# Performance work log

Measured on AMD Instinct MI355X. Metric: run time of the kernel, lower is better.

## Reference

```python
import jax, jax.numpy as jnp
import numpy as np

N, E = 50000, 800000
IN, HID, OUT, H = 128, 16, 16, 4


def setup_inputs() -> dict:
    key = jax.random.key(0)
    ks = jax.random.split(key, 11)
    sc = 0.1
    return {
        "features": jax.random.normal(ks[0], (N, IN), jnp.float32),
        "src": jax.random.randint(ks[1], (E,), 0, N, dtype=jnp.int64) if jax.config.jax_enable_x64 else jax.random.randint(ks[1], (E,), 0, N).astype(jnp.int32),
        "dst": jax.random.randint(ks[2], (E,), 0, N).astype(jnp.int32),
        "W1": jax.random.normal(ks[3], (H * HID, IN), jnp.float32) * sc,
        "al1": jax.random.normal(ks[4], (H, HID), jnp.float32) * sc,
        "ar1": jax.random.normal(ks[5], (H, HID), jnp.float32) * sc,
        "b1": jax.random.normal(ks[6], (H * HID,), jnp.float32) * sc,
        "W2": jax.random.normal(ks[7], (H * OUT, H * HID), jnp.float32) * sc,
        "al2": jax.random.normal(ks[8], (H, OUT), jnp.float32) * sc,
        "ar2": jax.random.normal(ks[9], (H, OUT), jnp.float32) * sc,
        "b2": jax.random.normal(ks[10], (H * OUT,), jnp.float32) * sc,
    }


def gat_conv(src, dst, feat, W, al, ar, b, heads, dout):
    """DGL-style GATConv: fc -> edge attention -> dst-softmax -> scatter-sum."""
    n = feat.shape[0]
    h = (feat @ W.T).reshape(n, heads, dout)            # [N,H,D]
    el = jnp.einsum("nhd,hd->nh", h, al)                # [N,H]
    er = jnp.einsum("nhd,hd->nh", h, ar)                # [N,H]
    e = jax.nn.leaky_relu(el[src] + er[dst], 0.2)       # [E,H]
    m = jax.ops.segment_max(e, dst, num_segments=n)     # per-dst max, [N,H]
    a = jnp.exp(e - m[dst])                             # [E,H]
    s = jax.ops.segment_sum(a, dst, num_segments=n)     # [N,H]
    alpha = a / s[dst]                                  # edge softmax, [E,H]
    out = jax.ops.segment_sum(alpha[:, :, None] * h[src], dst, num_segments=n)
    return out + b.reshape(1, heads, dout)              # [N,H,D]


def reference(features, src, dst, W1, al1, ar1, b1, W2, al2, ar2, b2):
    h = gat_conv(src, dst, features, W1, al1, ar1, b1, H, HID).reshape(N, H * HID)
    h = jax.nn.relu(h)
    h = gat_conv(src, dst, h, W2, al2, ar2, b2, H, OUT).mean(axis=1)  # mean over heads
    return jax.nn.log_softmax(h, axis=1)
```

## Files before the change

kernel.cpp:

```cpp
#include <hip/hip_runtime.h>
#include <math.h>

#define N_NODES 50000
#define N_EDGES 800000
#define NPART 8
#define PART_SZ ((N_NODES + NPART - 1) / NPART)
#define CAP 64
#define SCAT_BLOCKS 4096

typedef __attribute__((ext_vector_type(8))) short short8;
typedef __attribute__((ext_vector_type(8))) unsigned short ushort8;
typedef __attribute__((ext_vector_type(4))) float v4f;
typedef __attribute__((ext_vector_type(2))) float v2f;
typedef __attribute__((ext_vector_type(4))) int int4v;

__device__ __forceinline__ float bf2f(unsigned short h) {
    return __uint_as_float(((unsigned int)h) << 16);
}
__device__ __forceinline__ unsigned short f2bf(float f) {
    unsigned int u = __float_as_uint(f);
    u += 0x7fff + ((u >> 16) & 1);
    return (unsigned short)(u >> 16);
}

__device__ __forceinline__ short8 load_afrag(const float* X, size_t row, int K,
                                             int kc, int quad) {
    const float* p = X + row * K + kc * 32 + quad * 8;
    const float4 t0 = *(const float4*)p;
    const float4 t1 = *(const float4*)(p + 4);
    short8 a;
    a[0] = (short)f2bf(t0.x); a[1] = (short)f2bf(t0.y);
    a[2] = (short)f2bf(t0.z); a[3] = (short)f2bf(t0.w);
    a[4] = (short)f2bf(t1.x); a[5] = (short)f2bf(t1.y);
    a[6] = (short)f2bf(t1.z); a[7] = (short)f2bf(t1.w);
    return a;
}
__device__ __forceinline__ short8 load_afrag(const unsigned short* X, size_t row,
                                             int K, int kc, int quad) {
    return *(const short8*)(X + row * K + kc * 32 + quad * 8);
}

template <int K, typename XT>
__global__ __launch_bounds__(256) void fc_att_mfma(
    const XT* __restrict__ X, const float* __restrict__ W,
    const float* __restrict__ al, const float* __restrict__ ar,
    unsigned short* __restrict__ Hout, float* __restrict__ el,
    float* __restrict__ er, int nTiles)
{
    constexpr int KP = K + 4;
    constexpr int NKC = K / 32;
    __shared__ float Wlds[64 * KP];
    const int tid = threadIdx.x;
    for (int i = tid; i < 64 * K; i += 256) {
        int r = i / K, c = i - r * K;
        Wlds[r * KP + c] = W[i];
    }
    __syncthreads();

    const int lane = tid & 63;
    const int wave = tid >> 6;
    const int d = lane & 15;
    const int quad = lane >> 4;

    short8 wf[4][NKC];
#pragma unroll
    for (int ng = 0; ng < 4; ++ng) {
#pragma unroll
        for (int kc = 0; kc < NKC; ++kc) {
            const float* wp = &Wlds[(ng * 16 + d) * KP + kc * 32 + quad * 8];
            const v4f w0 = *(const v4f*)wp;
            const v4f w1 = *(const v4f*)(wp + 4);
            short8 f;
            f[0] = (short)f2bf(w0[0]); f[1] = (short)f2bf(w0[1]);
            f[2] = (short)f2bf(w0[2]); f[3] = (short)f2bf(w0[3]);
            f[4] = (short)f2bf(w1[0]); f[5] = (short)f2bf(w1[1]);
            f[6] = (short)f2bf(w1[2]); f[7] = (short)f2bf(w1[3]);
            wf[ng][kc] = f;
        }
    }

    const int tile = blockIdx.x * 4 + wave;
    if (tile >= nTiles) return;
    const int node0 = tile * 16;

    v4f cc[4] = {{0.f,0.f,0.f,0.f},{0.f,0.f,0.f,0.f},{0.f,0.f,0.f,0.f},{0.f,0.f,0.f,0.f}};
#pragma unroll
    for (int kc = 0; kc < NKC; ++kc) {
        const short8 a = load_afrag(X, (size_t)(node0 + d), K, kc, quad);
        cc[0] = __builtin_amdgcn_mfma_f32_16x16x32_bf16(a, wf[0][kc], cc[0], 0, 0, 0);
        cc[1] = __builtin_amdgcn_mfma_f32_16x16x32_bf16(a, wf[1][kc], cc[1], 0, 0, 0);
        cc[2] = __builtin_amdgcn_mfma_f32_16x16x32_bf16(a, wf[2][kc], cc[2], 0, 0, 0);
        cc[3] = __builtin_amdgcn_mfma_f32_16x16x32_bf16(a, wf[3][kc], cc[3], 0, 0, 0);
    }

#pragma unroll
    for (int ng = 0; ng < 4; ++ng) {
        const float alv = al[ng * 16 + d];
        const float arv = ar[ng * 16 + d];
        const v4f c = cc[ng];
#pragma unroll
        for (int r = 0; r < 4; ++r) {
            const int node = node0 + quad * 4 + r;
            Hout[(size_t)node * 64 + ng * 16 + d] = f2bf(c[r]);
            float vel = c[r] * alv;
            float ver = c[r] * arv;
#pragma unroll
            for (int off = 1; off < 16; off <<= 1) {
                vel += __shfl_xor(vel, off);
                ver += __shfl_xor(ver, off);
            }
            if (d == 0) {
                el[node * 4 + ng] = vel;
                er[node * 4 + ng] = ver;
            }
        }
    }
}

__device__ __forceinline__ void scat1(int d, int s, int lo, int hi,
                                      int* __restrict__ cnt16,
                                      unsigned short* __restrict__ col)
{
    if (d >= lo && d < hi) {
        const int pos = atomicAdd(&cnt16[(unsigned)d * 16], 1);
        if (pos < CAP) col[(unsigned)d * CAP + pos] = (unsigned short)s;
    }
}

__global__ __launch_bounds__(256) void scatter_bucket_kernel(
    const int* __restrict__ src, const int* __restrict__ dst,
    int* __restrict__ cnt16, unsigned short* __restrict__ col)
{
    const int part = blockIdx.x & (NPART - 1);
    const int lo = part * PART_SZ;
    const int hi = lo + PART_SZ;
    const int tid_p = ((int)blockIdx.x >> 3) * 256 + threadIdx.x;
    const int stride = (SCAT_BLOCKS / NPART) * 256;
    const int4v* dst4 = (const int4v*)dst;
    const int4v* src4 = (const int4v*)src;
    const int NQ = N_EDGES / 4;
    for (int q = tid_p; q < NQ; q += 2 * stride) {
        const int q2 = q + stride;
        const bool ok2 = q2 < NQ;
        const int4v dA = __builtin_nontemporal_load(dst4 + q);
        const int4v sA = __builtin_nontemporal_load(src4 + q);
        const int4v dB = ok2 ? __builtin_nontemporal_load(dst4 + q2) : (int4v){-1,-1,-1,-1};
        const int4v sB = ok2 ? __builtin_nontemporal_load(src4 + q2) : (int4v){0,0,0,0};
        scat1(dA[0], sA[0], lo, hi, cnt16, col);
        scat1(dA[1], sA[1], lo, hi, cnt16, col);
        scat1(dA[2], sA[2], lo, hi, cnt16, col);
        scat1(dA[3], sA[3], lo, hi, cnt16, col);
        scat1(dB[0], sB[0], lo, hi, cnt16, col);
        scat1(dB[1], sB[1], lo, hi, cnt16, col);
        scat1(dB[2], sB[2], lo, hi, cnt16, col);
        scat1(dB[3], sB[3], lo, hi, cnt16, col);
    }
}

__device__ __forceinline__ void agg_walk_pair(
    const unsigned short* __restrict__ colrow, int len, int len_max,
    const float* __restrict__ el, const unsigned int* __restrict__ Hf32,
    int hb, int hl, float erv_a,
    float& accL_out, float& accH_out, float& sacc_a_out)
{
    const int j_a = hl >> 2;
    const unsigned h_a = (unsigned)(hl & 3);
    const int hd = hl >> 3;
    float accL0 = 0.f, accL1 = 0.f, accH0 = 0.f, accH1 = 0.f;
    float sacc_a = 0.f;
    for (int i = 0; i < len_max; i += 16) {
        const ushort8 sv0 = __builtin_nontemporal_load((const ushort8*)(colrow + i));
        const ushort8 sv1 = __builtin_nontemporal_load((const ushort8*)(colrow + i + 8));
        const int rm = len - i;
        const unsigned sa0 = (unsigned)colrow[i + j_a];
        const unsigned sa1 = (unsigned)colrow[i + 8 + j_a];
        float x0 = el[sa0 * 4u + h_a] + erv_a;
        float x1 = el[sa1 * 4u + h_a] + erv_a;
        x0 = fmaxf(x0, 0.2f * x0);
        x1 = fmaxf(x1, 0.2f * x1);
        float a0 = __expf(x0);
        float a1 = __expf(x1);
        a0 = (j_a < rm) ? a0 : 0.f;
        a1 = (j_a + 8 < rm) ? a1 : 0.f;
        sacc_a += a0 + a1;
        unsigned uu[16];
#pragma unroll
        for (int j = 0; j < 8; ++j)
            uu[j] = Hf32[(unsigned)sv0[j] * 32u + (unsigned)hl];
#pragma unroll
        for (int j = 0; j < 8; ++j)
            uu[8 + j] = Hf32[(unsigned)sv1[j] * 32u + (unsigned)hl];
#pragma unroll
        for (int j = 0; j < 8; ++j) {
            const float aj = __shfl(a0, hb + j * 4 + hd);
            const float lo = __uint_as_float(uu[j] << 16);
            const float hi = __uint_as_float(uu[j] & 0xffff0000u);
            if (j & 1) { accL1 = fmaf(aj, lo, accL1); accH1 = fmaf(aj, hi, accH1); }
            else       { accL0 = fmaf(aj, lo, accL0); accH0 = fmaf(aj, hi, accH0); }
        }
#pragma unroll
        for (int j = 0; j < 8; ++j) {
            const float aj = __shfl(a1, hb + j * 4 + hd);
            const float lo = __uint_as_float(uu[8 + j] << 16);
            const float hi = __uint_as_float(uu[8 + j] & 0xffff0000u);
            if (j & 1) { accL1 = fmaf(aj, lo, accL1); accH1 = fmaf(aj, hi, accH1); }
            else       { accL0 = fmaf(aj, lo, accL0); accH0 = fmaf(aj, hi, accH0); }
        }
    }
    sacc_a += __shfl_xor(sacc_a, 4);
    sacc_a += __shfl_xor(sacc_a, 8);
    sacc_a += __shfl_xor(sacc_a, 16);
    sacc_a_out = sacc_a;
    accL_out = accL0 + accL1;
    accH_out = accH0 + accH1;
}

__global__ __launch_bounds__(256) void agg_relu_kernel(
    const int* __restrict__ cnt16, const unsigned short* __restrict__ col,
    const float* __restrict__ el, const float* __restrict__ er,
    const unsigned int* __restrict__ Hf32, const float* __restrict__ b,
    unsigned int* __restrict__ out32, int n)
{
    const int lane = threadIdx.x & 63;
    const int wave = threadIdx.x >> 6;
    const int hl = lane & 31;
    const int hb = lane & 32;
    const int node = blockIdx.x * 8 + wave * 2 + (lane >> 5);
    if (node >= n) return;
    const int hd = hl >> 3;
    const int cg = hd * 16 + (hl & 7) * 2;
    const float erv_a = er[node * 4 + (hl & 3)];
    const int len = min(cnt16[(unsigned)node * 16], CAP);
    const int len_max = max(len, __shfl_xor(len, 32));
    float accL, accH, sacc_a;
    agg_walk_pair(col + (unsigned)node * CAP, len, len_max, el, Hf32,
                  hb, hl, erv_a, accL, accH, sacc_a);
    const float sc = __shfl(sacc_a, hb + hd);
    float vL = sc > 0.f ? accL / sc : 0.f;
    float vH = sc > 0.f ? accH / sc : 0.f;
    vL += b[cg];   vH += b[cg + 1];
    vL = vL > 0.f ? vL : 0.f;
    vH = vH > 0.f ? vH : 0.f;
    const unsigned u = (unsigned)f2bf(vL) | ((unsigned)f2bf(vH) << 16);
    __builtin_nontemporal_store(u, out32 + (size_t)node * 32 + hl);
}

__global__ __launch_bounds__(256) void agg_final_kernel(
    const int* __restrict__ cnt16, const unsigned short* __restrict__ col,
    const float* __restrict__ el, const float* __restrict__ er,
    const unsigned int* __restrict__ Hf32, const float* __restrict__ b,
    float* __restrict__ out, int n)
{
    const int lane = threadIdx.x & 63;
    const int wave = threadIdx.x >> 6;
    const int hl = lane & 31;
    const int hb = lane & 32;
    const int node = blockIdx.x * 8 + wave * 2 + (lane >> 5);
    if (node >= n) return;
    const int hd = hl >> 3;
    const int cg = hd * 16 + (hl & 7) * 2;
    const float erv_a = er[node * 4 + (hl & 3)];
    const int len = min(cnt16[(unsigned)node * 16], CAP);
    const int len_max = max(len, __shfl_xor(len, 32));
    float accL, accH, sacc_a;
    agg_walk_pair(col + (unsigned)node * CAP, len, len_max, el, Hf32,
                  hb, hl, erv_a, accL, accH, sacc_a);
    const float sc = __shfl(sacc_a, hb + hd);
    float zL = sc > 0.f ? accL / sc : 0.f;
    float zH = sc > 0.f ? accH / sc : 0.f;
    zL += b[cg];   zH += b[cg + 1];
    zL += __shfl_xor(zL, 8);  zL += __shfl_xor(zL, 16);  zL *= 0.25f;
    zH += __shfl_xor(zH, 8);  zH += __shfl_xor(zH, 16);  zH *= 0.25f;
    float m = fmaxf(zL, zH);
    m = fmaxf(m, __shfl_xor(m, 1));
    m = fmaxf(m, __shfl_xor(m, 2));
    m = fmaxf(m, __shfl_xor(m, 4));
    float se = __expf(zL - m) + __expf(zH - m);
    se += __shfl_xor(se, 1);
    se += __shfl_xor(se, 2);
    se += __shfl_xor(se, 4);
    const float lse = __logf(se);
    if (hl < 8) {
        v2f r;
        r[0] = zL - m - lse;
        r[1] = zH - m - lse;
        __builtin_nontemporal_store(r, (v2f*)(out + (size_t)node * 16 + hl * 2));
    }
}

extern "C" void kernel_launch(void* const* d_in, const int* in_sizes, int n_in,
                              void* d_out, int out_size, void* d_ws, size_t ws_size,
                              hipStream_t stream)
{
    const float* feat = (const float*)d_in[0];
    const int*   src  = (const int*)d_in[1];
    const int*   dst  = (const int*)d_in[2];
    const float* W1   = (const float*)d_in[3];
    const float* al1  = (const float*)d_in[4];
    const float* ar1  = (const float*)d_in[5];
    const float* b1   = (const float*)d_in[6];
    const float* W2   = (const float*)d_in[7];
    const float* al2  = (const float*)d_in[8];
    const float* ar2  = (const float*)d_in[9];
    const float* b2   = (const float*)d_in[10];
    float* out = (float*)d_out;

    float* el  = (float*)d_ws;
    float* er  = el + N_NODES * 4;
    int*   cnt16 = (int*)(er + N_NODES * 4);
    uintptr_t p = ((uintptr_t)(cnt16 + N_NODES * 16) + 15) & ~(uintptr_t)15;
    unsigned short* col = (unsigned short*)p;
    unsigned short* A   = col + (size_t)N_NODES * CAP + 64;
    unsigned short* B   = A + (size_t)N_NODES * 64;

    const int NT = N_NODES / 16;
    const int FB = (NT + 3) / 4;
    const int AB2 = (N_NODES + 7) / 8;

    (void)hipMemsetAsync(cnt16, 0, (size_t)((char*)A - (char*)cnt16), stream);
    scatter_bucket_kernel<<<SCAT_BLOCKS, 256, 0, stream>>>(src, dst, cnt16, col);

    fc_att_mfma<128, float><<<FB, 256, 0, stream>>>(feat, W1, al1, ar1, A, el, er, NT);
    agg_relu_kernel<<<AB2, 256, 0, stream>>>(cnt16, col, el, er,
                                             (const unsigned int*)A, b1,
                                             (unsigned int*)B, N_NODES);

    fc_att_mfma<64, unsigned short><<<FB, 256, 0, stream>>>(B, W2, al2, ar2, A, el, er, NT);
    agg_final_kernel<<<AB2, 256, 0, stream>>>(cnt16, col, el, er,
                                              (const unsigned int*)A, b2, out, N_NODES);
}
```

Baseline: 197.8 us.

## Fuse layer-1 FC matmul and edge bucketing into one heterogeneous launch

Merges the edge scatter/bucketing kernel and the first FC+attention MFMA kernel into a single launch, where the first 784 blocks do the matmul and the rest do scatter. The two are independent, so this lets the compute-bound FC overlap with the atomic-heavy scatter and removes one launch gap. The weight tile is also stored in shared memory as bf16 instead of fp32 and is read straight into fragments, with no per-wave conversion. The trade-off is that the scatter blocks now reserve the FC shared-memory allocation, which may lower their occupancy.

```diff
diff --git a/kernel.cpp b/kernel.cpp
--- a/kernel.cpp
+++ b/kernel.cpp
@@ -7,6 +7,7 @@
 #define PART_SZ ((N_NODES + NPART - 1) / NPART)
 #define CAP 64
 #define SCAT_BLOCKS 4096
+#define FC_BLOCKS 784
 
 typedef __attribute__((ext_vector_type(8))) short short8;
 typedef __attribute__((ext_vector_type(8))) unsigned short ushort8;
@@ -41,19 +42,18 @@
 }
 
 template <int K, typename XT>
-__global__ __launch_bounds__(256) void fc_att_mfma(
+__device__ __forceinline__ void fc_att_body(
     const XT* __restrict__ X, const float* __restrict__ W,
     const float* __restrict__ al, const float* __restrict__ ar,
     unsigned short* __restrict__ Hout, float* __restrict__ el,
-    float* __restrict__ er, int nTiles)
-{
-    constexpr int KP = K + 4;
+    float* __restrict__ er, int nTiles, int blk, unsigned short* Wlds)
+{
+    constexpr int KP = K + 8;
     constexpr int NKC = K / 32;
-    __shared__ float Wlds[64 * KP];
     const int tid = threadIdx.x;
     for (int i = tid; i < 64 * K; i += 256) {
-        int r = i / K, c = i - r * K;
-        Wlds[r * KP + c] = W[i];
+        const int r = i / K, c = i - r * K;
+        Wlds[r * KP + c] = f2bf(W[i]);
     }
     __syncthreads();
 
@@ -62,26 +62,18 @@
     const int d = lane & 15;
     const int quad = lane >> 4;
 
-    short8 wf[4][NKC];
-#pragma unroll
-    for (int ng = 0; ng < 4; ++ng) {
-#pragma unroll
-        for (int kc = 0; kc < NKC; ++kc) {
-            const float* wp = &Wlds[(ng * 16 + d) * KP + kc * 32 + quad * 8];
-            const v4f w0 = *(const v4f*)wp;
-            const v4f w1 = *(const v4f*)(wp + 4);
-            short8 f;
-            f[0] = (short)f2bf(w0[0]); f[1] = (short)f2bf(w0[1]);
-            f[2] = (short)f2bf(w0[2]); f[3] = (short)f2bf(w0[3]);
-            f[4] = (short)f2bf(w1[0]); f[5] = (short)f2bf(w1[1]);
-            f[6] = (short)f2bf(w1[2]); f[7] = (short)f2bf(w1[3]);
-            wf[ng][kc] = f;
-        }
-    }
-
-    const int tile = blockIdx.x * 4 + wave;
+    const int tile = blk * 4 + wave;
     if (tile >= nTiles) return;
     const int node0 = tile * 16;
+
+    short8 wf[4][NKC];
+#pragma unroll
+    for (int ng = 0; ng < 4; ++ng) {
+#pragma unroll
+        for (int kc = 0; kc < NKC; ++kc) {
+            wf[ng][kc] = *(const short8*)&Wlds[(ng * 16 + d) * KP + kc * 32 + quad * 8];
+        }
+    }
 
     v4f cc[4] = {{0.f,0.f,0.f,0.f},{0.f,0.f,0.f,0.f},{0.f,0.f,0.f,0.f},{0.f,0.f,0.f,0.f}};
 #pragma unroll
@@ -117,6 +109,17 @@
     }
 }
 
+template <int K, typename XT>
+__global__ __launch_bounds__(256) void fc_att_mfma(
+    const XT* __restrict__ X, const float* __restrict__ W,
+    const float* __restrict__ al, const float* __restrict__ ar,
+    unsigned short* __restrict__ Hout, float* __restrict__ el,
+    float* __restrict__ er, int nTiles)
+{
+    __shared__ __align__(16) unsigned short Wlds[64 * (K + 8)];
+    fc_att_body<K, XT>(X, W, al, ar, Hout, el, er, nTiles, (int)blockIdx.x, Wlds);
+}
+
 __device__ __forceinline__ void scat1(int d, int s, int lo, int hi,
                                       int* __restrict__ cnt16,
                                       unsigned short* __restrict__ col)
@@ -127,33 +130,44 @@
     }
 }
 
-__global__ __launch_bounds__(256) void scatter_bucket_kernel(
+__global__ __launch_bounds__(256) void l1_fused_kernel(
+    const float* __restrict__ X, const float* __restrict__ W,
+    const float* __restrict__ al, const float* __restrict__ ar,
+    unsigned short* __restrict__ Hout, float* __restrict__ el,
+    float* __restrict__ er,
     const int* __restrict__ src, const int* __restrict__ dst,
     int* __restrict__ cnt16, unsigned short* __restrict__ col)
 {
-    const int part = blockIdx.x & (NPART - 1);
-    const int lo = part * PART_SZ;
-    const int hi = lo + PART_SZ;
-    const int tid_p = ((int)blockIdx.x >> 3) * 256 + threadIdx.x;
-    const int stride = (SCAT_BLOCKS / NPART) * 256;
-    const int4v* dst4 = (const int4v*)dst;
-    const int4v* src4 = (const int4v*)src;
-    const int NQ = N_EDGES / 4;
-    for (int q = tid_p; q < NQ; q += 2 * stride) {
-        const int q2 = q + stride;
-        const bool ok2 = q2 < NQ;
-        const int4v dA = __builtin_nontemporal_load(dst4 + q);
-        const int4v sA = __builtin_nontemporal_load(src4 + q);
-        const int4v dB = ok2 ? __builtin_nontemporal_load(dst4 + q2) : (int4v){-1,-1,-1,-1};
-        const int4v sB = ok2 ? __builtin_nontemporal_load(src4 + q2) : (int4v){0,0,0,0};
-        scat1(dA[0], sA[0], lo, hi, cnt16, col);
-        scat1(dA[1], sA[1], lo, hi, cnt16, col);
-        scat1(dA[2], sA[2], lo, hi, cnt16, col);
-        scat1(dA[3], sA[3], lo, hi, cnt16, col);
-        scat1(dB[0], sB[0], lo, hi, cnt16, col);
-        scat1(dB[1], sB[1], lo, hi, cnt16, col);
-        scat1(dB[2], sB[2], lo, hi, cnt16, col);
-        scat1(dB[3], sB[3], lo, hi, cnt16, col);
+    __shared__ __align__(16) unsigned short Wlds[64 * (128 + 8)];
+    if ((int)blockIdx.x < FC_BLOCKS) {
+        fc_att_body<128, float>(X, W, al, ar, Hout, el, er,
+                                N_NODES / 16, (int)blockIdx.x, Wlds);
+    } else {
+        const int bid = (int)blockIdx.x - FC_BLOCKS;
+        const int part = bid & (NPART - 1);
+        const int lo = part * PART_SZ;
+        const int hi = lo + PART_SZ;
+        const int tid_p = (bid >> 3) * 256 + (int)threadIdx.x;
+        const int stride = (SCAT_BLOCKS / NPART) * 256;
+        const int4v* dst4 = (const int4v*)dst;
+        const int4v* src4 = (const int4v*)src;
+        const int NQ = N_EDGES / 4;
+        for (int q = tid_p; q < NQ; q += 2 * stride) {
+            const int q2 = q + stride;
+            const bool ok2 = q2 < NQ;
+            const int4v dA = __builtin_nontemporal_load(dst4 + q);
+            const int4v sA = __builtin_nontemporal_load(src4 + q);
+            const int4v dB = ok2 ? __builtin_nontemporal_load(dst4 + q2) : (int4v){-1,-1,-1,-1};
+            const int4v sB = ok2 ? __builtin_nontemporal_load(src4 + q2) : (int4v){0,0,0,0};
+            scat1(dA[0], sA[0], lo, hi, cnt16, col);
+            scat1(dA[1], sA[1], lo, hi, cnt16, col);
+            scat1(dA[2], sA[2], lo, hi, cnt16, col);
+            scat1(dA[3], sA[3], lo, hi, cnt16, col);
+            scat1(dB[0], sB[0], lo, hi, cnt16, col);
+            scat1(dB[1], sB[1], lo, hi, cnt16, col);
+            scat1(dB[2], sB[2], lo, hi, cnt16, col);
+            scat1(dB[3], sB[3], lo, hi, cnt16, col);
+        }
     }
 }
 
@@ -318,9 +332,9 @@
     const int AB2 = (N_NODES + 7) / 8;
 
     (void)hipMemsetAsync(cnt16, 0, (size_t)((char*)A - (char*)cnt16), stream);
-    scatter_bucket_kernel<<<SCAT_BLOCKS, 256, 0, stream>>>(src, dst, cnt16, col);
-
-    fc_att_mfma<128, float><<<FB, 256, 0, stream>>>(feat, W1, al1, ar1, A, el, er, NT);
+
+    l1_fused_kernel<<<FC_BLOCKS + SCAT_BLOCKS, 256, 0, stream>>>(
+        feat, W1, al1, ar1, A, el, er, src, dst, cnt16, col);
     agg_relu_kernel<<<AB2, 256, 0, stream>>>(cnt16, col, el, er,
                                              (const unsigned int*)A, b1,
                                              (unsigned int*)B, N_NODES);
```

Result: faster. 185.9 us (-6.0%).
